# Kernel tuning notes

Measured on AMD Instinct MI355X. Metric: run time of the kernel, lower is better.

## Reference

```python
import jax, jax.numpy as jnp
import numpy as np

N, E, D, ED, G = 50000, 800000, 64, 32, 50


def setup_inputs() -> dict:
    key = jax.random.key(0)
    ks = jax.random.split(key, 24)
    s = 0.05
    inp = {
        "x": jax.random.normal(ks[0], (N, D), jnp.float32),
        "edge_attr": jax.random.normal(ks[1], (E, ED), jnp.float32),
        "edge_index": jax.random.randint(ks[2], (2, E), 0, N, jnp.int64),
    }
    i = 3
    for step in range(2):
        inp[f"fe{step}_W1"] = jax.random.normal(ks[i], (2 * D + ED, D), jnp.float32) * s; i += 1
        inp[f"fe{step}_b1"] = jnp.zeros((D,), jnp.float32)
        inp[f"fe{step}_W2"] = jax.random.normal(ks[i], (D, D), jnp.float32) * s; i += 1
        inp[f"fe{step}_b2"] = jnp.zeros((D,), jnp.float32)
        inp[f"lstm{step}_Wih"] = jax.random.normal(ks[i], (D, 4 * D), jnp.float32) * s; i += 1
        inp[f"lstm{step}_Whh"] = jax.random.normal(ks[i], (D, 4 * D), jnp.float32) * s; i += 1
        inp[f"lstm{step}_bih"] = jnp.zeros((4 * D,), jnp.float32)
        inp[f"lstm{step}_bhh"] = jnp.zeros((4 * D,), jnp.float32)
    inp["gm_W"] = jax.random.normal(ks[i], (D, G), jnp.float32) * s; i += 1
    inp["gm_b"] = jnp.zeros((G,), jnp.float32)
    inp["fm_W"] = jax.random.normal(ks[i], (D, G), jnp.float32) * s; i += 1
    inp["fm_b"] = jnp.zeros((G,), jnp.float32)
    return inp


def _mpn(x, edge_attr, src, dst, W1, b1, W2, b2):
    # x_i = x[dst] (target), x_j = x[src] (source); aggregate 'add' at dst
    m = jnp.concatenate([x[dst], x[src], edge_attr], axis=1)  # [E, 2D+ED]
    m = jax.nn.relu(m @ W1 + b1) @ W2 + b2                    # [E, D]
    return jax.ops.segment_sum(m, dst, num_segments=x.shape[0])


def _lstm_cell(inp, h, c, Wih, Whh, bih, bhh):
    gates = inp @ Wih + h @ Whh + (bih + bhh)  # [N, 4D], gate order i,f,g,o
    i, f, g, o = jnp.split(gates, 4, axis=1)
    c = jax.nn.sigmoid(f) * c + jax.nn.sigmoid(i) * jnp.tanh(g)
    h = jax.nn.sigmoid(o) * jnp.tanh(c)
    return h, c


def reference(x, edge_attr, edge_index,
              fe0_W1, fe0_b1, fe0_W2, fe0_b2,
              lstm0_Wih, lstm0_Whh, lstm0_bih, lstm0_bhh,
              fe1_W1, fe1_b1, fe1_W2, fe1_b2,
              lstm1_Wih, lstm1_Whh, lstm1_bih, lstm1_bhh,
              gm_W, gm_b, fm_W, fm_b):
    src, dst = edge_index[0], edge_index[1]
    c = jnp.zeros_like(x)
    fes = [(fe0_W1, fe0_b1, fe0_W2, fe0_b2), (fe1_W1, fe1_b1, fe1_W2, fe1_b2)]
    lstms = [(lstm0_Wih, lstm0_Whh, lstm0_bih, lstm0_bhh),
             (lstm1_Wih, lstm1_Whh, lstm1_bih, lstm1_bhh)]
    for step in range(2):
        a = _mpn(x, edge_attr, src, dst, *fes[step])
        # LSTMCell(input=x, (h=a, c=c)) as in the original forward
        x, c = _lstm_cell(x, a, c, *lstms[step])
    g = jax.nn.sigmoid(x @ gm_W + gm_b)   # [N, G]
    h_v_G = x @ fm_W + fm_b               # [N, G]
    return jnp.sum(g * h_v_G, axis=0)     # [G]
```

## Files before the change

### kernel.cpp

```cpp
#include <hip/hip_runtime.h>
#include <hip/hip_bf16.h>

using short8 = __attribute__((ext_vector_type(8))) short;
using f32x4  = __attribute__((ext_vector_type(4))) float;

#define KLP 136

__device__ __forceinline__ unsigned short f2bf(float f) {
  unsigned u = __float_as_uint(f);
  u += 0x7FFFu + ((u >> 16) & 1u);
  return (unsigned short)(u >> 16);
}
__device__ __forceinline__ unsigned pack2(float a, float b) {
  return (unsigned)f2bf(a) | ((unsigned)f2bf(b) << 16);
}
#if __has_builtin(__builtin_amdgcn_rcpf)
__device__ __forceinline__ float fast_rcp(float x) { return __builtin_amdgcn_rcpf(x); }
#else
__device__ __forceinline__ float fast_rcp(float x) { return 1.f / x; }
#endif
__device__ __forceinline__ float sigm(float x) { return fast_rcp(1.f + __expf(-x)); }
__device__ __forceinline__ float tanh_f(float x) { return fmaf(2.f, sigm(2.f * x), -1.f); }

__global__ __launch_bounds__(256) void prep_all(
    const float* __restrict__ x,
    const float* __restrict__ W1_0, const float* __restrict__ Wih0,
    const float* __restrict__ bih0, const float* __restrict__ bhh0,
    const float* __restrict__ W1_1, const float* __restrict__ Wih1,
    const float* __restrict__ bih1, const float* __restrict__ bhh1,
    const float* __restrict__ W2_0, const float* __restrict__ Whh0, const float* __restrict__ b2_0,
    const float* __restrict__ W2_1, const float* __restrict__ Whh1, const float* __restrict__ b2_1,
    const float* __restrict__ gmW, const float* __restrict__ fmW,
    unsigned short* __restrict__ W1T,
    unsigned short* __restrict__ WcT,
    float* __restrict__ bG,
    float* __restrict__ b2h,
    unsigned short* __restrict__ WrT,
    unsigned short* __restrict__ xb0,
    float* __restrict__ aggrH,
    int* __restrict__ histA,
    float* __restrict__ outZ, int nOut,
    int N)
{
  int t = blockIdx.x * 256 + threadIdx.x;

  const int R0 = 2 * 26880 + 8192;
  if (t < R0) {
    const int per = 26880;
    if (t >= 2 * per) {
      int r2 = t - 2 * per;
      int o = r2 >> 6, k = r2 & 63;
      float v = 0.f;
      if (o < 50) v = gmW[k * 50 + o];
      else if (o >= 64 && o < 114) v = fmW[k * 50 + (o - 64)];
      WrT[o * 64 + k] = f2bf(v);
      return;
    }
    int step = t / per, r = t % per;
    const float* W1  = step ? W1_1 : W1_0;
    const float* Wih = step ? Wih1 : Wih0;
    const float* bih = step ? bih1 : bih0;
    const float* bhh = step ? bhh1 : bhh0;
    if (r < 10240) {
      int o = r / 160, k = r % 160;
      W1T[step * 10240 + o * 160 + k] = f2bf(W1[k * 64 + o]);
    } else if (r < 26624) {
      int rr = r - 10240;
      int g = rr >> 6, k = rr & 63;
      WcT[step * 32768 + g * 128 + k] = f2bf(Wih[k * 256 + g]);
    } else {
      int g = r - 26624;
      bG[step * 256 + g] = bih[g] + bhh[g];
    }
    return;
  }
  t -= R0;

  const int R1 = 33280;
  if (t < R1) {
    if (t < 32768) {
      int step = t >> 14, r = t & 16383;
      int g = r >> 6, k = r & 63;
      const float* W2  = step ? W2_1 : W2_0;
      const float* Whh = step ? Whh1 : Whh0;
      float v = 0.f;
      for (int j = 0; j < 64; ++j) v = fmaf(W2[k * 64 + j], Whh[j * 256 + g], v);
      WcT[step * 32768 + g * 128 + 64 + k] = f2bf(v);
    } else {
      int r = t - 32768;
      int step = r >> 8, g = r & 255;
      const float* b2  = step ? b2_1 : b2_0;
      const float* Whh = step ? Whh1 : Whh0;
      float v = 0.f;
      for (int j = 0; j < 64; ++j) v = fmaf(b2[j], Whh[j * 256 + g], v);
      b2h[step * 256 + g] = v;
    }
    return;
  }
  t -= R1;

  const int R2 = N * 8;
  if (t < R2) {
    const float4* p = (const float4*)(x + (long long)t * 8);
    float4 a0 = p[0], a1 = p[1];
    *(uint4*)(xb0 + (long long)t * 8) =
        make_uint4(pack2(a0.x, a0.y), pack2(a0.z, a0.w), pack2(a1.x, a1.y), pack2(a1.z, a1.w));
    return;
  }
  t -= R2;

  const int R3 = N * 16;
  if (t < R3) { ((float4*)aggrH)[t] = make_float4(0.f, 0.f, 0.f, 0.f); return; }
  t -= R3;

  const int R4 = N / 4;
  if (t < R4) { ((int4*)histA)[t] = make_int4(0, 0, 0, 0); return; }
  t -= R4;

  if (t < nOut) outZ[t] = 0.f;
}

__global__ __launch_bounds__(256) void hist_kernel(
    const int* __restrict__ dstI, int* __restrict__ hist, int E)
{
  int e = blockIdx.x * 256 + threadIdx.x;
  if (e < E) atomicAdd(&hist[dstI[e]], 1);
}

__global__ __launch_bounds__(256) void scan_part(
    const int* __restrict__ hist, int2* __restrict__ blockTot, int N)
{
  __shared__ int sD[256], sS[256];
  int t = threadIdx.x;
  int n = blockIdx.x * 256 + t;
  int d = (n < N) ? hist[n] : 0;
  int sg = (d + 15) >> 4;
  sD[t] = d; sS[t] = sg;
  __syncthreads();
  #pragma unroll
  for (int off = 128; off; off >>= 1) {
    if (t < off) { sD[t] += sD[t + off]; sS[t] += sS[t + off]; }
    __syncthreads();
  }
  if (t == 0) blockTot[blockIdx.x] = make_int2(sD[0], sS[0]);
}

__global__ __launch_bounds__(256) void scan_mid(
    const int2* __restrict__ blockTot, int2* __restrict__ blockBase,
    int* __restrict__ nSegTot, int nb)
{
  __shared__ int sD[256], sS[256];
  int t = threadIdx.x;
  int d = 0, s = 0;
  if (t < nb) { int2 v = blockTot[t]; d = v.x; s = v.y; }
  sD[t] = d; sS[t] = s;
  __syncthreads();
  #pragma unroll
  for (int off = 1; off < 256; off <<= 1) {
    int vd = (t >= off) ? sD[t - off] : 0;
    int vs = (t >= off) ? sS[t - off] : 0;
    __syncthreads();
    sD[t] += vd; sS[t] += vs;
    __syncthreads();
  }
  if (t < nb) blockBase[t] = make_int2(sD[t] - d, sS[t] - s);
  if (t == nb - 1) *nSegTot = sS[t];
}

__global__ __launch_bounds__(256) void scan_final(
    const int* __restrict__ hist, const int2* __restrict__ blockBase,
    int* __restrict__ cursor, int4* __restrict__ segInfo, int N)
{
  __shared__ int sD[256], sS[256];
  int t = threadIdx.x;
  int n = blockIdx.x * 256 + t;
  int d = (n < N) ? hist[n] : 0;
  int sg = (d + 15) >> 4;
  sD[t] = d; sS[t] = sg;
  __syncthreads();
  #pragma unroll
  for (int off = 1; off < 256; off <<= 1) {
    int vd = (t >= off) ? sD[t - off] : 0;
    int vs = (t >= off) ? sS[t - off] : 0;
    __syncthreads();
    sD[t] += vd; sS[t] += vs;
    __syncthreads();
  }
  if (n < N) {
    int2 bb = blockBase[blockIdx.x];
    int degBase = bb.x + sD[t] - d;
    int segBase = bb.y + sS[t] - sg;
    cursor[n] = degBase;
    for (int j = 0; j < sg; ++j)
      segInfo[segBase + j] = make_int4(degBase + j * 16, n, min(d - j * 16, 16), 0);
  }
}

__global__ __launch_bounds__(256) void scatter_perm(
    const int* __restrict__ srcI, const int* __restrict__ dstI,
    const float* __restrict__ ea, int* __restrict__ cursor,
    int* __restrict__ srcS, unsigned short* __restrict__ eaS, int E)
{
  int e = blockIdx.x * 256 + threadIdx.x;
  if (e >= E) return;
  int d = dstI[e];
  int p = atomicAdd(&cursor[d], 1);
  srcS[p] = srcI[e];
  const float4* pe = (const float4*)(ea + (long long)e * 32);
  float4 a0 = pe[0], a1 = pe[1], a2 = pe[2], a3 = pe[3];
  float4 a4 = pe[4], a5 = pe[5], a6 = pe[6], a7 = pe[7];
  uint4* out = (uint4*)(eaS + (long long)p * 32);
  out[0] = make_uint4(pack2(a0.x, a0.y), pack2(a0.z, a0.w), pack2(a1.x, a1.y), pack2(a1.z, a1.w));
  out[1] = make_uint4(pack2(a2.x, a2.y), pack2(a2.z, a2.w), pack2(a3.x, a3.y), pack2(a3.z, a3.w));
  out[2] = make_uint4(pack2(a4.x, a4.y), pack2(a4.z, a4.w), pack2(a5.x, a5.y), pack2(a5.z, a5.w));
  out[3] = make_uint4(pack2(a6.x, a6.y), pack2(a6.z, a6.w), pack2(a7.x, a7.y), pack2(a7.z, a7.w));
}

__global__ __launch_bounds__(256) void edge_gemm(
    const unsigned short* __restrict__ xb,
    const unsigned short* __restrict__ eaS,
    const int* __restrict__ srcS,
    const int4* __restrict__ segInfo,
    const int* __restrict__ nSegPtr,
    const unsigned short* __restrict__ W1T,
    const float* __restrict__ b1,
    float* __restrict__ aggrH)
{
  __shared__ unsigned short stash[20 * 64 * 8];
  const int t = threadIdx.x;
  const int w = t >> 6, l = t & 63;
  const int quad = l >> 4, lr = l & 15;

  #pragma unroll
  for (int p = 0; p < 5; ++p) {
    int idx = p * 256 + t;
    int grp = idx >> 6, ll = idx & 63;
    int kc = grp >> 2, n = grp & 3;
    *(uint4*)(stash + idx * 8) =
        *(const uint4*)(W1T + (n * 16 + (ll & 15)) * 160 + kc * 32 + (ll >> 4) * 8);
  }
  float bb[4];
  #pragma unroll
  for (int n = 0; n < 4; ++n) bb[n] = b1[n * 16 + lr];
  __syncthreads();

  const int nSeg = *nSegPtr;
  const int W = gridDim.x * 4;
  int s = blockIdx.x * 4 + w;
  if (s >= nSeg) return;
  int4 si = segInfo[s];
  int src = srcS[si.x + min(lr, si.z - 1)];

  while (true) {
    const int sn = s + W;
    const bool more = sn < nSeg;
    int4 si_n = si;
    if (more) si_n = segInfo[sn];

    const int start = si.x, node = si.y, cnt = si.z;
    const int er = min(lr, cnt - 1);

    const short8* pd = (const short8*)(xb + (long long)node * 64);
    const short8* ps = (const short8*)(xb + (long long)src * 64);
    short8 a0 = pd[quad];
    short8 a1 = pd[4 + quad];
    short8 a2 = ps[quad];
    short8 a3 = ps[4 + quad];
    short8 a4 = *(const short8*)(eaS + (long long)(start + er) * 32 + quad * 8);

    int src_n = src;
    if (more) src_n = srcS[si_n.x + min(lr, si_n.z - 1)];

    f32x4 acc[4] = {};
    #pragma unroll
    for (int kc = 0; kc < 5; ++kc) {
      short8 aX = (kc == 0) ? a0 : (kc == 1) ? a1 : (kc == 2) ? a2 : (kc == 3) ? a3 : a4;
      #pragma unroll
      for (int n = 0; n < 4; ++n) {
        short8 bFr = *(const short8*)(stash + (((kc << 2) | n) * 64 + l) * 8);
        acc[n] = __builtin_amdgcn_mfma_f32_16x16x32_bf16(aX, bFr, acc[n], 0, 0, 0);
      }
    }

    float myv = 0.f;
    #pragma unroll
    for (int n = 0; n < 4; ++n) {
      float sum = 0.f;
      #pragma unroll
      for (int rr = 0; rr < 4; ++rr) {
        float v = fmaxf(acc[n][rr] + bb[n], 0.f);
        sum += (quad * 4 + rr < cnt) ? v : 0.f;
      }
      sum += __shfl_xor(sum, 16);
      sum += __shfl_xor(sum, 32);
      if (quad == n) myv = sum;
    }
    unsafeAtomicAdd(&aggrH[(long long)node * 64 + l], myv);

    if (!more) break;
    s = sn; si = si_n; src = src_n;
  }
}

__global__ __launch_bounds__(256) void lstm3(
    const unsigned short* __restrict__ xbin,
    float* __restrict__ aggrH,
    const float* __restrict__ cin,
    float* __restrict__ cout,
    const unsigned short* __restrict__ WcT,
    const float* __restrict__ bG,
    const float* __restrict__ b2h,
    const int* __restrict__ degA,
    unsigned short* __restrict__ xbout,
    int nNodes, int zeroAggr)
{
  __shared__ unsigned short sIn[64 * KLP];
  __shared__ unsigned short sW[64 * KLP];
  __shared__ float sBG[256], sB2h[256];
  const int t = threadIdx.x;
  sBG[t] = bG[t];
  sB2h[t] = b2h[t];

  const int base_n = blockIdx.x * 64;
  const int nl = t >> 2, q = t & 3;
  const int node = base_n + nl;
  unsigned short* rowp = sIn + nl * KLP;
  if (node < nNodes) {
    const uint4* px = (const uint4*)(xbin + (long long)node * 64);
    *(uint4*)(rowp + q * 16)     = px[q * 2];
    *(uint4*)(rowp + q * 16 + 8) = px[q * 2 + 1];
    float4* pg = (float4*)(aggrH + (long long)node * 64) + q * 4;
    float4 g0 = pg[0], g1 = pg[1], g2 = pg[2], g3 = pg[3];
    *(uint4*)(rowp + 64 + q * 16) =
        make_uint4(pack2(g0.x, g0.y), pack2(g0.z, g0.w), pack2(g1.x, g1.y), pack2(g1.z, g1.w));
    *(uint4*)(rowp + 64 + q * 16 + 8) =
        make_uint4(pack2(g2.x, g2.y), pack2(g2.z, g2.w), pack2(g3.x, g3.y), pack2(g3.z, g3.w));
    if (zeroAggr) {
      float4 z = make_float4(0.f, 0.f, 0.f, 0.f);
      pg[0] = z; pg[1] = z; pg[2] = z; pg[3] = z;
    }
  } else {
    *(uint4*)(rowp + q * 16)          = make_uint4(0, 0, 0, 0);
    *(uint4*)(rowp + q * 16 + 8)      = make_uint4(0, 0, 0, 0);
    *(uint4*)(rowp + 64 + q * 16)     = make_uint4(0, 0, 0, 0);
    *(uint4*)(rowp + 64 + q * 16 + 8) = make_uint4(0, 0, 0, 0);
  }

  const int w = t >> 6, l = t & 63, quad = l >> 4, lr = l & 15;
  const int row0 = w * 16;
  f32x4 acc[16] = {};
  for (int grp = 0; grp < 4; ++grp) {
    const uint4* gw = (const uint4*)WcT + (long long)(grp * 64) * 16;
    uint4* lw = (uint4*)sW;
    {
      int o0 = t >> 4, s4 = t & 15;
      #pragma unroll
      for (int pp = 0; pp < 4; ++pp) {
        int o = pp * 16 + o0;
        lw[o * 17 + s4] = gw[o * 16 + s4];
      }
    }
    __syncthreads();
    #pragma unroll
    for (int kc = 0; kc < 4; ++kc) {
      short8 aF = *(const short8*)(sIn + (row0 + lr) * KLP + kc * 32 + quad * 8);
      #pragma unroll
      for (int nt = 0; nt < 4; ++nt) {
        short8 bF = *(const short8*)(sW + (nt * 16 + lr) * KLP + kc * 32 + quad * 8);
        acc[grp * 4 + nt] = __builtin_amdgcn_mfma_f32_16x16x32_bf16(aF, bF, acc[grp * 4 + nt], 0, 0, 0);
      }
    }
    __syncthreads();
  }

  #pragma unroll
  for (int nt = 0; nt < 4; ++nt) {
    #pragma unroll
    for (int rr = 0; rr < 4; ++rr) {
      int node2 = base_n + row0 + quad * 4 + rr;
      if (node2 < nNodes) {
        int col = nt * 16 + lr;
        long long off = (long long)node2 * 64 + col;
        float dg = (float)degA[node2];
        float iv = acc[nt][rr]      + sBG[col]       + dg * sB2h[col];
        float fv = acc[4 + nt][rr]  + sBG[64 + col]  + dg * sB2h[64 + col];
        float gv = acc[8 + nt][rr]  + sBG[128 + col] + dg * sB2h[128 + col];
        float ov = acc[12 + nt][rr] + sBG[192 + col] + dg * sB2h[192 + col];
        float cOld = cin ? cin[off] : 0.f;
        float cN = sigm(fv) * cOld + sigm(iv) * tanh_f(gv);
        float hN = sigm(ov) * tanh_f(cN);
        cout[off] = cN;
        xbout[off] = f2bf(hN);
      }
    }
  }
}

__global__ __launch_bounds__(256) void readout(
    const unsigned short* __restrict__ xq,
    const unsigned short* __restrict__ WrT,
    const float* __restrict__ gb, const float* __restrict__ fb,
    float* __restrict__ out, int nNodes)
{
  __shared__ unsigned short sX[64 * 72];
  __shared__ unsigned short sW[128 * 72];
  __shared__ float sOut[4][64];
  __shared__ float sGb[64], sFb[64];
  const int t = threadIdx.x;
  {
    const uint4* gw = (const uint4*)WrT;
    uint4* lw = (uint4*)sW;
    #pragma unroll
    for (int pp = 0; pp < 4; ++pp) {
      int idx = t + pp * 256;
      int o = idx >> 3, s = idx & 7;
      lw[o * 9 + s] = gw[idx];
    }
    if (t < 50)      { sGb[t] = gb[t]; sFb[t] = fb[t]; }
    else if (t < 64) { sGb[t] = 0.f;   sFb[t] = 0.f; }
  }
  const int base = blockIdx.x * 64;
  const int nl = t >> 2, q = t & 3;
  const int node = base + nl;
  {
    uint4* dst = (uint4*)(sX + nl * 72 + q * 16);
    if (node < nNodes) {
      const uint4* px = (const uint4*)(xq + (long long)node * 64);
      dst[0] = px[q * 2];
      dst[1] = px[q * 2 + 1];
    } else {
      dst[0] = make_uint4(0, 0, 0, 0);
      dst[1] = make_uint4(0, 0, 0, 0);
    }
  }
  __syncthreads();

  const int w = t >> 6, l = t & 63, quad = l >> 4, lr = l & 15;
  f32x4 acc[8] = {};
  #pragma unroll
  for (int kc = 0; kc < 2; ++kc) {
    short8 aF = *(const short8*)(sX + (w * 16 + lr) * 72 + kc * 32 + quad * 8);
    #pragma unroll
    for (int n = 0; n < 8; ++n) {
      short8 bF = *(const short8*)(sW + (n * 16 + lr) * 72 + kc * 32 + quad * 8);
      acc[n] = __builtin_amdgcn_mfma_f32_16x16x32_bf16(aF, bF, acc[n], 0, 0, 0);
    }
  }
  #pragma unroll
  for (int n = 0; n < 4; ++n) {
    float val = 0.f;
    #pragma unroll
    for (int rr = 0; rr < 4; ++rr) {
      int nd = base + w * 16 + quad * 4 + rr;
      if (nd < nNodes) {
        int jj = n * 16 + lr;
        float gv = sigm(acc[n][rr] + sGb[jj]);
        float fv = acc[n + 4][rr] + sFb[jj];
        val += gv * fv;
      }
    }
    val += __shfl_xor(val, 16);
    val += __shfl_xor(val, 32);
    if (quad == 0) sOut[w][n * 16 + lr] = val;
  }
  __syncthreads();
  if (t < 50) {
    float s = sOut[0][t] + sOut[1][t] + sOut[2][t] + sOut[3][t];
    unsafeAtomicAdd(&out[t], s);
  }
}

extern "C" void kernel_launch(void* const* d_in, const int* in_sizes, int n_in,
                              void* d_out, int out_size, void* d_ws, size_t ws_size,
                              hipStream_t stream)
{
  const float* x      = (const float*)d_in[0];
  const float* ea     = (const float*)d_in[1];
  const int*   ei     = (const int*)d_in[2];
  const float* fe0_W1 = (const float*)d_in[3];
  const float* fe0_b1 = (const float*)d_in[4];
  const float* fe0_W2 = (const float*)d_in[5];
  const float* fe0_b2 = (const float*)d_in[6];
  const float* l0_Wih = (const float*)d_in[7];
  const float* l0_Whh = (const float*)d_in[8];
  const float* l0_bih = (const float*)d_in[9];
  const float* l0_bhh = (const float*)d_in[10];
  const float* fe1_W1 = (const float*)d_in[11];
  const float* fe1_b1 = (const float*)d_in[12];
  const float* fe1_W2 = (const float*)d_in[13];
  const float* fe1_b2 = (const float*)d_in[14];
  const float* l1_Wih = (const float*)d_in[15];
  const float* l1_Whh = (const float*)d_in[16];
  const float* l1_bih = (const float*)d_in[17];
  const float* l1_bhh = (const float*)d_in[18];
  const float* gm_W   = (const float*)d_in[19];
  const float* gm_b   = (const float*)d_in[20];
  const float* fm_W   = (const float*)d_in[21];
  const float* fm_b   = (const float*)d_in[22];

  const int N = in_sizes[0] / 64;
  const int E = in_sizes[1] / 32;
  const int* srcI = ei;
  const int* dstI = ei + E;

  char* ws = (char*)d_ws;
  unsigned short* xb0     = (unsigned short*)(ws + 0);
  unsigned short* xb1     = (unsigned short*)(ws + 6400000);
  float*          aggrH   = (float*)(ws + 12800000);
  float*          cbuf    = (float*)(ws + 25600000);
  unsigned short* eaS     = (unsigned short*)(ws + 38400000);
  int*            srcS    = (int*)(ws + 89601024);
  int4*           segInfo = (int4*)(ws + 92801088);
  int*            histA   = (int*)(ws + 94401280);
  int*            curA    = (int*)(ws + 94601280);
  unsigned short* W1T     = (unsigned short*)(ws + 94801280);
  unsigned short* WcT     = (unsigned short*)(ws + 94842240);
  float*          bG      = (float*)(ws + 94973312);
  float*          b2h     = (float*)(ws + 94975360);
  unsigned short* WrT     = (unsigned short*)(ws + 94977408);
  int*            nSegPtr = (int*)(ws + 94993792);
  int2*           blockTot  = (int2*)(ws + 94993856);
  int2*           blockBase = (int2*)(ws + 94995904);

  const int prepT = (2 * 26880 + 8192) + 33280 + N * 8 + N * 16 + N / 4 + out_size;
  prep_all<<<(prepT + 255) / 256, 256, 0, stream>>>(
      x,
      fe0_W1, l0_Wih, l0_bih, l0_bhh,
      fe1_W1, l1_Wih, l1_bih, l1_bhh,
      fe0_W2, l0_Whh, fe0_b2,
      fe1_W2, l1_Whh, fe1_b2,
      gm_W, fm_W,
      W1T, WcT, bG, b2h, WrT, xb0,
      aggrH, histA, (float*)d_out, out_size, N);

  const int nb = (N + 255) / 256;
  hist_kernel<<<(E + 255) / 256, 256, 0, stream>>>(dstI, histA, E);
  scan_part<<<nb, 256, 0, stream>>>(histA, blockTot, N);
  scan_mid<<<1, 256, 0, stream>>>(blockTot, blockBase, nSegPtr, nb);
  scan_final<<<nb, 256, 0, stream>>>(histA, blockBase, curA, segInfo, N);
  scatter_perm<<<(E + 255) / 256, 256, 0, stream>>>(srcI, dstI, ea, curA, srcS, eaS, E);

  const int nodeBlocks = (N + 63) / 64;

  edge_gemm<<<2048, 256, 0, stream>>>(xb0, eaS, srcS, segInfo, nSegPtr,
                                      W1T, fe0_b1, aggrH);
  lstm3<<<nodeBlocks, 256, 0, stream>>>(xb0, aggrH, nullptr, cbuf, WcT, bG, b2h,
                                        histA, xb1, N, 1);

  edge_gemm<<<2048, 256, 0, stream>>>(xb1, eaS, srcS, segInfo, nSegPtr,
                                      W1T + 10240, fe1_b1, aggrH);
  lstm3<<<nodeBlocks, 256, 0, stream>>>(xb1, aggrH, cbuf, cbuf, WcT + 32768,
                                        bG + 256, b2h + 256, histA, xb0, N, 0);

  readout<<<nodeBlocks, 256, 0, stream>>>(xb0, WrT, gm_b, fm_b, (float*)d_out, N);
}
```

Before: 452.2 us.

## Convert edge attributes to bf16 in place and gather via permutation index

Edge attributes are now cast to bf16 in original edge order inside the prep kernel, so the cast is a coalesced streaming pass. The scatter kernel no longer copies attribute rows into dst-sorted order; it only records an edge permutation index. The edge GEMM then gathers each attribute row through that index. This replaces a scattered 64-byte write per edge with an extra index load and non-contiguous attribute reads in both edge GEMM passes.

```diff
diff --git a/kernel.cpp b/kernel.cpp
--- a/kernel.cpp
+++ b/kernel.cpp
@@ -24,6 +24,7 @@
 
 __global__ __launch_bounds__(256) void prep_all(
     const float* __restrict__ x,
+    const float* __restrict__ ea,
     const float* __restrict__ W1_0, const float* __restrict__ Wih0,
     const float* __restrict__ bih0, const float* __restrict__ bhh0,
     const float* __restrict__ W1_1, const float* __restrict__ Wih1,
@@ -37,10 +38,11 @@
     float* __restrict__ b2h,
     unsigned short* __restrict__ WrT,
     unsigned short* __restrict__ xb0,
+    unsigned short* __restrict__ eaB,
     float* __restrict__ aggrH,
     int* __restrict__ histA,
     float* __restrict__ outZ, int nOut,
-    int N)
+    int N, int E4)
 {
   int t = blockIdx.x * 256 + threadIdx.x;
 
@@ -117,7 +119,15 @@
   if (t < R4) { ((int4*)histA)[t] = make_int4(0, 0, 0, 0); return; }
   t -= R4;
 
-  if (t < nOut) outZ[t] = 0.f;
+  if (t < nOut) { outZ[t] = 0.f; return; }
+  t -= nOut;
+
+  if (t < E4) {
+    const float4* p = (const float4*)(ea + (long long)t * 8);
+    float4 a0 = p[0], a1 = p[1];
+    *(uint4*)(eaB + (long long)t * 8) =
+        make_uint4(pack2(a0.x, a0.y), pack2(a0.z, a0.w), pack2(a1.x, a1.y), pack2(a1.z, a1.w));
+  }
 }
 
 __global__ __launch_bounds__(256) void hist_kernel(
@@ -196,29 +206,23 @@
   }
 }
 
-__global__ __launch_bounds__(256) void scatter_perm(
+__global__ __launch_bounds__(256) void perm_build(
     const int* __restrict__ srcI, const int* __restrict__ dstI,
-    const float* __restrict__ ea, int* __restrict__ cursor,
-    int* __restrict__ srcS, unsigned short* __restrict__ eaS, int E)
+    int* __restrict__ cursor, int* __restrict__ ePerm,
+    int* __restrict__ srcS, int E)
 {
   int e = blockIdx.x * 256 + threadIdx.x;
   if (e >= E) return;
   int d = dstI[e];
   int p = atomicAdd(&cursor[d], 1);
+  ePerm[p] = e;
   srcS[p] = srcI[e];
-  const float4* pe = (const float4*)(ea + (long long)e * 32);
-  float4 a0 = pe[0], a1 = pe[1], a2 = pe[2], a3 = pe[3];
-  float4 a4 = pe[4], a5 = pe[5], a6 = pe[6], a7 = pe[7];
-  uint4* out = (uint4*)(eaS + (long long)p * 32);
-  out[0] = make_uint4(pack2(a0.x, a0.y), pack2(a0.z, a0.w), pack2(a1.x, a1.y), pack2(a1.z, a1.w));
-  out[1] = make_uint4(pack2(a2.x, a2.y), pack2(a2.z, a2.w), pack2(a3.x, a3.y), pack2(a3.z, a3.w));
-  out[2] = make_uint4(pack2(a4.x, a4.y), pack2(a4.z, a4.w), pack2(a5.x, a5.y), pack2(a5.z, a5.w));
-  out[3] = make_uint4(pack2(a6.x, a6.y), pack2(a6.z, a6.w), pack2(a7.x, a7.y), pack2(a7.z, a7.w));
 }
 
 __global__ __launch_bounds__(256) void edge_gemm(
     const unsigned short* __restrict__ xb,
-    const unsigned short* __restrict__ eaS,
+    const unsigned short* __restrict__ eaB,
+    const int* __restrict__ ePerm,
     const int* __restrict__ srcS,
     const int4* __restrict__ segInfo,
     const int* __restrict__ nSegPtr,
@@ -249,7 +253,9 @@
   int s = blockIdx.x * 4 + w;
   if (s >= nSeg) return;
   int4 si = segInfo[s];
-  int src = srcS[si.x + min(lr, si.z - 1)];
+  int pos = si.x + min(lr, si.z - 1);
+  int src = srcS[pos];
+  int ep  = ePerm[pos];
 
   while (true) {
     const int sn = s + W;
@@ -257,8 +263,7 @@
     int4 si_n = si;
     if (more) si_n = segInfo[sn];
 
-    const int start = si.x, node = si.y, cnt = si.z;
-    const int er = min(lr, cnt - 1);
+    const int node = si.y, cnt = si.z;
 
     const short8* pd = (const short8*)(xb + (long long)node * 64);
     const short8* ps = (const short8*)(xb + (long long)src * 64);
@@ -266,10 +271,14 @@
     short8 a1 = pd[4 + quad];
     short8 a2 = ps[quad];
     short8 a3 = ps[4 + quad];
-    short8 a4 = *(const short8*)(eaS + (long long)(start + er) * 32 + quad * 8);
-
-    int src_n = src;
-    if (more) src_n = srcS[si_n.x + min(lr, si_n.z - 1)];
+    short8 a4 = *(const short8*)(eaB + (long long)ep * 32 + quad * 8);
+
+    int src_n = src, ep_n = ep;
+    if (more) {
+      int pos_n = si_n.x + min(lr, si_n.z - 1);
+      src_n = srcS[pos_n];
+      ep_n  = ePerm[pos_n];
+    }
 
     f32x4 acc[4] = {};
     #pragma unroll
@@ -298,7 +307,7 @@
     unsafeAtomicAdd(&aggrH[(long long)node * 64 + l], myv);
 
     if (!more) break;
-    s = sn; si = si_n; src = src_n;
+    s = sn; si = si_n; src = src_n; ep = ep_n;
   }
 }
 
@@ -508,7 +517,7 @@
   unsigned short* xb1     = (unsigned short*)(ws + 6400000);
   float*          aggrH   = (float*)(ws + 12800000);
   float*          cbuf    = (float*)(ws + 25600000);
-  unsigned short* eaS     = (unsigned short*)(ws + 38400000);
+  unsigned short* eaB     = (unsigned short*)(ws + 38400000);
   int*            srcS    = (int*)(ws + 89601024);
   int4*           segInfo = (int4*)(ws + 92801088);
   int*            histA   = (int*)(ws + 94401280);
@@ -521,33 +530,35 @@
   int*            nSegPtr = (int*)(ws + 94993792);
   int2*           blockTot  = (int2*)(ws + 94993856);
   int2*           blockBase = (int2*)(ws + 94995904);
-
-  const int prepT = (2 * 26880 + 8192) + 33280 + N * 8 + N * 16 + N / 4 + out_size;
+  int*            ePerm   = (int*)(ws + 95000000);
+
+  const int E4 = E * 4;
+  const int prepT = (2 * 26880 + 8192) + 33280 + N * 8 + N * 16 + N / 4 + out_size + E4;
   prep_all<<<(prepT + 255) / 256, 256, 0, stream>>>(
-      x,
+      x, ea,
       fe0_W1, l0_Wih, l0_bih, l0_bhh,
       fe1_W1, l1_Wih, l1_bih, l1_bhh,
       fe0_W2, l0_Whh, fe0_b2,
       fe1_W2, l1_Whh, fe1_b2,
       gm_W, fm_W,
-      W1T, WcT, bG, b2h, WrT, xb0,
-      aggrH, histA, (float*)d_out, out_size, N);
+      W1T, WcT, bG, b2h, WrT, xb0, eaB,
+      aggrH, histA, (float*)d_out, out_size, N, E4);
 
   const int nb = (N + 255) / 256;
   hist_kernel<<<(E + 255) / 256, 256, 0, stream>>>(dstI, histA, E);
   scan_part<<<nb, 256, 0, stream>>>(histA, blockTot, N);
   scan_mid<<<1, 256, 0, stream>>>(blockTot, blockBase, nSegPtr, nb);
   scan_final<<<nb, 256, 0, stream>>>(histA, blockBase, curA, segInfo, N);
-  scatter_perm<<<(E + 255) / 256, 256, 0, stream>>>(srcI, dstI, ea, curA, srcS, eaS, E);
+  perm_build<<<(E + 255) / 256, 256, 0, stream>>>(srcI, dstI, curA, ePerm, srcS, E);
 
   const int nodeBlocks = (N + 63) / 64;
 
-  edge_gemm<<<2048, 256, 0, stream>>>(xb0, eaS, srcS, segInfo, nSegPtr,
+  edge_gemm<<<2048, 256, 0, stream>>>(xb0, eaB, ePerm, srcS, segInfo, nSegPtr,
                                       W1T, fe0_b1, aggrH);
   lstm3<<<nodeBlocks, 256, 0, stream>>>(xb0, aggrH, nullptr, cbuf, WcT, bG, b2h,
                                         histA, xb1, N, 1);
 
-  edge_gemm<<<2048, 256, 0, stream>>>(xb1, eaS, srcS, segInfo, nSegPtr,
+  edge_gemm<<<2048, 256, 0, stream>>>(xb1, eaB, ePerm, srcS, segInfo, nSegPtr,
                                       W1T + 10240, fe1_b1, aggrH);
   lstm3<<<nodeBlocks, 256, 0, stream>>>(xb1, aggrH, cbuf, cbuf, WcT + 32768,
                                         bG + 256, b2h + 256, histA, xb0, N, 0);
```

New measurement: 468.5 us. 1.04x slower.

## Fuse readout into final LSTM kernel and split edge scatter across four lanes

Applied to the files above, without the earlier changes.

The final LSTM step now keeps the new hidden state in shared memory and runs the readout GEMM, sigmoid gating and node reduction in the same kernel. This removes the separate readout launch and the write and re-read of the final hidden state and cell state. The edge-attribute scatter now uses four threads per edge, one of which does the atomic cursor bump and broadcasts the slot by shuffle, so each thread handles a 16-byte chunk. The risks are the reuse of the weight shared buffer at a different size and more shared-memory synchronisation in the LSTM kernel.

```diff
diff --git a/kernel.cpp b/kernel.cpp
--- a/kernel.cpp
+++ b/kernel.cpp
@@ -201,19 +201,22 @@
     const float* __restrict__ ea, int* __restrict__ cursor,
     int* __restrict__ srcS, unsigned short* __restrict__ eaS, int E)
 {
-  int e = blockIdx.x * 256 + threadIdx.x;
+  const int t = threadIdx.x;
+  const int l = t & 63;
+  const int e = blockIdx.x * 64 + (t >> 2);
+  const int c = t & 3;
   if (e >= E) return;
-  int d = dstI[e];
-  int p = atomicAdd(&cursor[d], 1);
-  srcS[p] = srcI[e];
-  const float4* pe = (const float4*)(ea + (long long)e * 32);
-  float4 a0 = pe[0], a1 = pe[1], a2 = pe[2], a3 = pe[3];
-  float4 a4 = pe[4], a5 = pe[5], a6 = pe[6], a7 = pe[7];
-  uint4* out = (uint4*)(eaS + (long long)p * 32);
-  out[0] = make_uint4(pack2(a0.x, a0.y), pack2(a0.z, a0.w), pack2(a1.x, a1.y), pack2(a1.z, a1.w));
-  out[1] = make_uint4(pack2(a2.x, a2.y), pack2(a2.z, a2.w), pack2(a3.x, a3.y), pack2(a3.z, a3.w));
-  out[2] = make_uint4(pack2(a4.x, a4.y), pack2(a4.z, a4.w), pack2(a5.x, a5.y), pack2(a5.z, a5.w));
-  out[3] = make_uint4(pack2(a6.x, a6.y), pack2(a6.z, a6.w), pack2(a7.x, a7.y), pack2(a7.z, a7.w));
+  int p = 0;
+  if (c == 0) {
+    int d = dstI[e];
+    p = atomicAdd(&cursor[d], 1);
+    srcS[p] = srcI[e];
+  }
+  p = __shfl(p, l & ~3);
+  const float4* pe = (const float4*)(ea + (long long)e * 32 + c * 8);
+  float4 a0 = pe[0], a1 = pe[1];
+  *(uint4*)(eaS + (long long)p * 32 + c * 8) =
+      make_uint4(pack2(a0.x, a0.y), pack2(a0.z, a0.w), pack2(a1.x, a1.y), pack2(a1.z, a1.w));
 }
 
 __global__ __launch_bounds__(256) void edge_gemm(
@@ -312,10 +315,13 @@
     const float* __restrict__ b2h,
     const int* __restrict__ degA,
     unsigned short* __restrict__ xbout,
-    int nNodes, int zeroAggr)
+    const unsigned short* __restrict__ WrT,
+    const float* __restrict__ gb, const float* __restrict__ fb,
+    float* __restrict__ outG,
+    int nNodes, int zeroAggr, int doReadout)
 {
   __shared__ unsigned short sIn[64 * KLP];
-  __shared__ unsigned short sW[64 * KLP];
+  __shared__ unsigned short sW[128 * 72];
   __shared__ float sBG[256], sB2h[256];
   const int t = threadIdx.x;
   sBG[t] = bG[t];
@@ -378,8 +384,9 @@
     #pragma unroll
     for (int rr = 0; rr < 4; ++rr) {
       int node2 = base_n + row0 + quad * 4 + rr;
+      int rl = row0 + quad * 4 + rr;
+      int col = nt * 16 + lr;
       if (node2 < nNodes) {
-        int col = nt * 16 + lr;
         long long off = (long long)node2 * 64 + col;
         float dg = (float)degA[node2];
         float iv = acc[nt][rr]      + sBG[col]       + dg * sB2h[col];
@@ -389,24 +396,21 @@
         float cOld = cin ? cin[off] : 0.f;
         float cN = sigm(fv) * cOld + sigm(iv) * tanh_f(gv);
         float hN = sigm(ov) * tanh_f(cN);
-        cout[off] = cN;
-        xbout[off] = f2bf(hN);
+        if (doReadout) {
+          sIn[rl * 72 + col] = f2bf(hN);
+        } else {
+          cout[off] = cN;
+          xbout[off] = f2bf(hN);
+        }
+      } else if (doReadout) {
+        sIn[rl * 72 + col] = 0;
       }
     }
   }
-}
-
-__global__ __launch_bounds__(256) void readout(
-    const unsigned short* __restrict__ xq,
-    const unsigned short* __restrict__ WrT,
-    const float* __restrict__ gb, const float* __restrict__ fb,
-    float* __restrict__ out, int nNodes)
-{
-  __shared__ unsigned short sX[64 * 72];
-  __shared__ unsigned short sW[128 * 72];
-  __shared__ float sOut[4][64];
-  __shared__ float sGb[64], sFb[64];
-  const int t = threadIdx.x;
+
+  if (!doReadout) return;
+
+  __syncthreads();
   {
     const uint4* gw = (const uint4*)WrT;
     uint4* lw = (uint4*)sW;
@@ -416,57 +420,45 @@
       int o = idx >> 3, s = idx & 7;
       lw[o * 9 + s] = gw[idx];
     }
-    if (t < 50)      { sGb[t] = gb[t]; sFb[t] = fb[t]; }
-    else if (t < 64) { sGb[t] = 0.f;   sFb[t] = 0.f; }
-  }
-  const int base = blockIdx.x * 64;
-  const int nl = t >> 2, q = t & 3;
-  const int node = base + nl;
-  {
-    uint4* dst = (uint4*)(sX + nl * 72 + q * 16);
-    if (node < nNodes) {
-      const uint4* px = (const uint4*)(xq + (long long)node * 64);
-      dst[0] = px[q * 2];
-      dst[1] = px[q * 2 + 1];
-    } else {
-      dst[0] = make_uint4(0, 0, 0, 0);
-      dst[1] = make_uint4(0, 0, 0, 0);
-    }
-  }
-  __syncthreads();
-
-  const int w = t >> 6, l = t & 63, quad = l >> 4, lr = l & 15;
-  f32x4 acc[8] = {};
+  }
+  if (t < 64) {
+    sBG[t]      = (t < 50) ? gb[t] : 0.f;
+    sBG[64 + t] = (t < 50) ? fb[t] : 0.f;
+  }
+  __syncthreads();
+
+  f32x4 racc[8] = {};
   #pragma unroll
   for (int kc = 0; kc < 2; ++kc) {
-    short8 aF = *(const short8*)(sX + (w * 16 + lr) * 72 + kc * 32 + quad * 8);
+    short8 aF = *(const short8*)(sIn + (w * 16 + lr) * 72 + kc * 32 + quad * 8);
     #pragma unroll
     for (int n = 0; n < 8; ++n) {
       short8 bF = *(const short8*)(sW + (n * 16 + lr) * 72 + kc * 32 + quad * 8);
-      acc[n] = __builtin_amdgcn_mfma_f32_16x16x32_bf16(aF, bF, acc[n], 0, 0, 0);
-    }
-  }
+      racc[n] = __builtin_amdgcn_mfma_f32_16x16x32_bf16(aF, bF, racc[n], 0, 0, 0);
+    }
+  }
+  float* sOutF = sB2h;
   #pragma unroll
   for (int n = 0; n < 4; ++n) {
     float val = 0.f;
     #pragma unroll
     for (int rr = 0; rr < 4; ++rr) {
-      int nd = base + w * 16 + quad * 4 + rr;
+      int nd = base_n + w * 16 + quad * 4 + rr;
       if (nd < nNodes) {
         int jj = n * 16 + lr;
-        float gv = sigm(acc[n][rr] + sGb[jj]);
-        float fv = acc[n + 4][rr] + sFb[jj];
+        float gv = sigm(racc[n][rr] + sBG[jj]);
+        float fv = racc[n + 4][rr] + sBG[64 + jj];
         val += gv * fv;
       }
     }
     val += __shfl_xor(val, 16);
     val += __shfl_xor(val, 32);
-    if (quad == 0) sOut[w][n * 16 + lr] = val;
+    if (quad == 0) sOutF[w * 64 + n * 16 + lr] = val;
   }
   __syncthreads();
   if (t < 50) {
-    float s = sOut[0][t] + sOut[1][t] + sOut[2][t] + sOut[3][t];
-    unsafeAtomicAdd(&out[t], s);
+    float sm = sOutF[t] + sOutF[64 + t] + sOutF[128 + t] + sOutF[192 + t];
+    unsafeAtomicAdd(&outG[t], sm);
   }
 }
 
@@ -538,19 +530,20 @@
   scan_part<<<nb, 256, 0, stream>>>(histA, blockTot, N);
   scan_mid<<<1, 256, 0, stream>>>(blockTot, blockBase, nSegPtr, nb);
   scan_final<<<nb, 256, 0, stream>>>(histA, blockBase, curA, segInfo, N);
-  scatter_perm<<<(E + 255) / 256, 256, 0, stream>>>(srcI, dstI, ea, curA, srcS, eaS, E);
+  scatter_perm<<<(E + 63) / 64, 256, 0, stream>>>(srcI, dstI, ea, curA, srcS, eaS, E);
 
   const int nodeBlocks = (N + 63) / 64;
 
   edge_gemm<<<2048, 256, 0, stream>>>(xb0, eaS, srcS, segInfo, nSegPtr,
                                       W1T, fe0_b1, aggrH);
   lstm3<<<nodeBlocks, 256, 0, stream>>>(xb0, aggrH, nullptr, cbuf, WcT, bG, b2h,
-                                        histA, xb1, N, 1);
+                                        histA, xb1, WrT, gm_b, fm_b, (float*)d_out,
+                                        N, 1, 0);
 
   edge_gemm<<<2048, 256, 0, stream>>>(xb1, eaS, srcS, segInfo, nSegPtr,
                                       W1T + 10240, fe1_b1, aggrH);
-  lstm3<<<nodeBlocks, 256, 0, stream>>>(xb1, aggrH, cbuf, cbuf, WcT + 32768,
-                                        bG + 256, b2h + 256, histA, xb0, N, 0);
-
-  readout<<<nodeBlocks, 256, 0, stream>>>(xb0, WrT, gm_b, fm_b, (float*)d_out, N);
-}
+  lstm3<<<nodeBlocks, 256, 0, stream>>>(xb1, aggrH, cbuf, nullptr, WcT + 32768,
+                                        bG + 256, b2h + 256, histA, nullptr,
+                                        WrT, gm_b, fm_b, (float*)d_out,
+                                        N, 0, 1);
+}
```

Measured after the change: 435.1 us. 3.8% less time.
